# Performance work log

Hardware: AMD Instinct MI355X
Metric: run time of the kernel (lower is better)

The kernel has to match this reference:

```python
import jax, jax.numpy as jnp
import numpy as np

B, N_PER, P_PER = 64, 64, 2016   # graphs, nodes/graph, pairs/graph (C(64,2))
IN_DIM, HID, OUT = 64, 128, 10
EDGE_P = 0.125


def _build_graph_structures():
    """Integer preprocessing replicating build_2sets_from_embeddings's
    combinatorics (pairs, iso_type source, triangle-based 2-set edges)."""
    rng = np.random.default_rng(0)
    n, b = N_PER, B
    A = rng.random((b, n, n)) < EDGE_P
    A = np.triu(A, 1)
    A = A | A.transpose(0, 2, 1)                      # symmetric, no self loops
    gs, us, vs = np.nonzero(A)                        # directed edges, both dirs
    edge_index = np.stack([gs * n + us, gs * n + vs]).astype(np.int64)
    batch = np.repeat(np.arange(b), n).astype(np.int64)
    iu, iv = np.triu_indices(n, 1)                    # local pair (u<v) lists
    pidx = np.full((n, n), -1, np.int64)
    pidx[iu, iv] = np.arange(P_PER)
    pidx[iv, iu] = np.arange(P_PER)                   # symmetric lookup = sorted()
    pair_u = (np.arange(b)[:, None] * n + iu[None, :]).ravel().astype(np.int64)
    pair_v = (np.arange(b)[:, None] * n + iv[None, :]).ravel().astype(np.int64)
    iso_type = A[:, iu, iv].astype(np.float32).ravel()[:, None]  # [B*P_PER,1]
    # 2-set edges: pair (u,v) -> sorted(v,w) and sorted(u,w) for every common
    # neighbor w of u and v (matches _build_2set_edges exactly)
    common = A[:, iu, :] & A[:, iv, :]                # (B, P_PER, n)
    g2, ps, ws = np.nonzero(common)
    u, v = iu[ps], iv[ps]
    d1 = pidx[v, ws]
    d2 = pidx[u, ws]
    src = np.concatenate([g2 * P_PER + ps, g2 * P_PER + ps])
    dst = np.concatenate([g2 * P_PER + d1, g2 * P_PER + d2])
    two_edges = np.stack([src, dst]).astype(np.int64)
    two_batch = np.repeat(np.arange(b), P_PER).astype(np.int64)
    return edge_index, batch, pair_u, pair_v, iso_type, two_edges, two_batch


def setup_inputs() -> dict:
    ei, batch, pu, pv, iso, te, tb = _build_graph_structures()
    key = jax.random.key(0)
    ks = jax.random.split(key, 16)
    w = lambda k, i, o: jax.random.normal(k, (i, o), jnp.float32) / np.float32(np.sqrt(i))
    two_in = 2 * HID + 1
    return {
        "x": jax.random.normal(ks[0], (B * N_PER, IN_DIM), jnp.float32),
        "g1_W1_0": w(ks[1], IN_DIM, HID), "g1_W2_0": w(ks[2], IN_DIM, HID),
        "g1_W1_1": w(ks[3], HID, HID),    "g1_W2_1": w(ks[4], HID, HID),
        "g1_W1_2": w(ks[5], HID, HID),    "g1_W2_2": w(ks[6], HID, HID),
        "k_W1_0": w(ks[7], two_in, HID),  "k_W2_0": w(ks[8], two_in, HID),
        "k_W1_1": w(ks[9], HID, HID),     "k_W2_1": w(ks[10], HID, HID),
        "c_W0": w(ks[11], 2 * HID, HID),  "c_b0": jnp.zeros((HID,), jnp.float32),
        "c_W1": w(ks[12], HID, OUT),      "c_b1": jnp.zeros((OUT,), jnp.float32),
        "iso_type": jnp.asarray(iso),
        "edge_index": jnp.asarray(ei), "batch": jnp.asarray(batch),
        "pair_u": jnp.asarray(pu), "pair_v": jnp.asarray(pv),
        "two_edges": jnp.asarray(te), "two_batch": jnp.asarray(tb),
    }


def _mp_layer(h, ei, W1, W2):
    # relu( h @ W1 + scatter_add_{dst}( h[src] @ W2 ) )  -- OneGNNLayer / KSetLayer
    msg = h[ei[0]] @ W2
    agg = jax.ops.segment_sum(msg, ei[1], num_segments=h.shape[0])
    return jax.nn.relu(h @ W1 + agg)


def reference(x, g1_W1_0, g1_W2_0, g1_W1_1, g1_W2_1, g1_W1_2, g1_W2_2,
              k_W1_0, k_W2_0, k_W1_1, k_W2_1,
              c_W0, c_b0, c_W1, c_b1,
              iso_type, edge_index, batch, pair_u, pair_v, two_edges, two_batch):
    h = _mp_layer(x, edge_index, g1_W1_0, g1_W2_0)
    h = _mp_layer(h, edge_index, g1_W1_1, g1_W2_1)
    h = _mp_layer(h, edge_index, g1_W1_2, g1_W2_2)
    graph_emb_1 = jax.ops.segment_sum(h, batch, num_segments=B)
    # 2-set features: [h_u, h_v, iso_type]  -> [P, 2H+1]
    two_x = jnp.concatenate([h[pair_u], h[pair_v], iso_type], axis=1)
    h2 = _mp_layer(two_x, two_edges, k_W1_0, k_W2_0)
    h2 = _mp_layer(h2, two_edges, k_W1_1, k_W2_1)
    graph_emb_2 = jax.ops.segment_sum(h2, two_batch, num_segments=B)
    combined = jnp.concatenate([graph_emb_1, graph_emb_2], axis=1)
    hc = jax.nn.relu(combined @ c_W0 + c_b0)   # Dropout(p=0.5) inactive in eval
    return hc @ c_W1 + c_b1
```

## Files before the change

kernel.cpp:

```cpp
#include <hip/hip_runtime.h>
#include <hip/hip_bf16.h>


typedef short s16x8 __attribute__((ext_vector_type(8)));
typedef float f32x4 __attribute__((ext_vector_type(4)));

__device__ __forceinline__ unsigned short f2bf(float f) {
  union { float f; unsigned u; } x; x.f = f;
  unsigned r = (x.u + 0x7fffu + ((x.u >> 16) & 1u)) >> 16;
  return (unsigned short)r;
}
__device__ __forceinline__ float bf2f(unsigned short h) {
  union { unsigned u; float f; } x; x.u = ((unsigned)h) << 16;
  return x.f;
}
__device__ __forceinline__ float4 ldbf4(const unsigned short* p) {
  ushort4 q = *(const ushort4*)p;
  return make_float4(bf2f(q.x), bf2f(q.y), bf2f(q.z), bf2f(q.w));
}
__device__ __forceinline__ void stbf4(unsigned short* p, float4 v) {
  ushort4 q;
  q.x = f2bf(v.x); q.y = f2bf(v.y); q.z = f2bf(v.z); q.w = f2bf(v.w);
  *(ushort4*)p = q;
}
__device__ __forceinline__ float4 ld4(const float* p) { return *(const float4*)p; }

template<int KCS, int ASTR>
__device__ __forceinline__ void mfma_dual_lds(
    const unsigned short* A, const unsigned short* Wfrag,
    f32x4 (&accA)[8], f32x4 (&accB)[8])
{
  const int lane = threadIdx.x & 63;
  const int wv = threadIdx.x >> 6;
  const int row = wv * 16 + (lane & 15);
  const int k0 = (lane >> 4) << 3;
  const unsigned short* ap = A + row * ASTR + k0;
  const unsigned short* wp = Wfrag + (size_t)lane * 8;
#pragma unroll
  for (int i = 0; i < 8; ++i) { accA[i] = (f32x4)0.f; accB[i] = (f32x4)0.f; }
#pragma unroll
  for (int kc = 0; kc < KCS; ++kc) {
    s16x8 af = *(const s16x8*)(ap + kc * 32);
#pragma unroll
    for (int nt = 0; nt < 8; ++nt) {
      s16x8 b0 = *(const s16x8*)(wp + ((size_t)((nt)*KCS + kc) << 9));
      s16x8 b1 = *(const s16x8*)(wp + ((size_t)((8 + nt) * KCS + kc) << 9));
      accA[nt] = __builtin_amdgcn_mfma_f32_16x16x32_bf16(af, b0, accA[nt], 0, 0, 0);
      accB[nt] = __builtin_amdgcn_mfma_f32_16x16x32_bf16(af, b1, accB[nt], 0, 0, 0);
    }
  }
}

__device__ __forceinline__ void epi_lds(const f32x4 (&accA)[8], const f32x4 (&accB)[8],
    unsigned short (*preS)[136], unsigned short (*msgS)[136])
{
  const int lane = threadIdx.x & 63;
  const int wv = threadIdx.x >> 6;
  const int col = lane & 15;
  const int r0 = wv * 16 + ((lane >> 4) << 2);
  __syncthreads();
#pragma unroll
  for (int nt = 0; nt < 8; ++nt)
#pragma unroll
    for (int r = 0; r < 4; ++r) {
      preS[r0 + r][nt * 16 + col] = f2bf(accA[nt][r]);
      msgS[r0 + r][nt * 16 + col] = f2bf(accB[nt][r]);
    }
  __syncthreads();
}

__device__ __forceinline__ void epi_global(const f32x4 (&accA)[8], const f32x4 (&accB)[8],
    unsigned short (*sOut)[136], unsigned short* Ca, unsigned short* Cb, long tile)
{
  const int tid = threadIdx.x;
  const int lane = tid & 63;
  const int wv = tid >> 6;
  const int col = lane & 15;
  const int r0 = wv * 16 + ((lane >> 4) << 2);
  const long rowBase = tile * 64;
#pragma unroll
  for (int sel = 0; sel < 2; ++sel) {
    __syncthreads();
#pragma unroll
    for (int nt = 0; nt < 8; ++nt) {
#pragma unroll
      for (int r = 0; r < 4; ++r)
        sOut[r0 + r][nt * 16 + col] = f2bf(sel ? accB[nt][r] : accA[nt][r]);
    }
    __syncthreads();
    unsigned short* C = sel ? Cb : Ca;
#pragma unroll
    for (int i = 0; i < 4; ++i) {
      int fi = tid + i * 256;
      int row = fi >> 4;
      int c8 = fi & 15;
      *(uint4*)(C + (rowBase + row) * 128 + c8 * 8) = *(uint4*)&sOut[row][c8 * 8];
    }
  }
}

struct NArgs {
  const float* x;
  const int* ei;
  const int* gstart;
  const unsigned short *Wf0, *Wf1, *Wf2, *Wf3, *Wf4;
  unsigned short *HU1, *HV1, *HU2, *HV2;
  float* ge1;
  int E1;
};

__global__ __launch_bounds__(256) void node_stage(NArgs a)
{
  __shared__ __align__(16) unsigned short hS[64][136];
  __shared__ __align__(16) unsigned short preS[64][136];
  __shared__ __align__(16) unsigned short msgS[64][136];
  __shared__ int ldeg[64], lcur[64], loff[65];
  __shared__ unsigned short ledge[1024];
  __shared__ float sge[128];

  const int b = blockIdx.x;
  const int t = threadIdx.x;
  const int base = b * 64;

  const int es = a.gstart[b], ee = a.gstart[b + 1];
  if (t < 64) ldeg[t] = 0;
  if (t < 128) sge[t] = 0.f;
  __syncthreads();
  for (int i = es + t; i < ee; i += 256)
    atomicAdd(&ldeg[a.ei[a.E1 + i] - base], 1);
  __syncthreads();
  if (t < 64) {
    int v = ldeg[t], s = v;
#pragma unroll
    for (int d = 1; d < 64; d <<= 1) {
      int o = __shfl_up(s, d, 64);
      if (t >= d) s += o;
    }
    loff[t] = s - v;
    lcur[t] = s - v;
    if (t == 63) loff[64] = s;
  }
  unsigned short* xs = &preS[0][0];
  for (int i = t; i < 64 * 64; i += 256) {
    int r = i >> 6, c = i & 63;
    xs[r * 72 + c] = f2bf(a.x[(size_t)(base + r) * 64 + c]);
  }
  __syncthreads();
  for (int i = es + t; i < ee; i += 256) {
    int s = a.ei[i] - base, d = a.ei[a.E1 + i] - base;
    int pos = atomicAdd(&lcur[d], 1);
    ledge[pos] = (unsigned short)s;
  }
  __syncthreads();

  f32x4 accA[8], accB[8];
  const int grp = t >> 5, f = (t & 31) * 4;

  mfma_dual_lds<2, 72>(xs, a.Wf0, accA, accB);
  epi_lds(accA, accB, preS, msgS);
  for (int r = grp; r < 64; r += 8) {
    float4 acc = ldbf4(&preS[r][f]);
    int j1 = loff[r + 1];
    for (int j = loff[r]; j < j1; ++j) {
      float4 m = ldbf4(&msgS[ledge[j]][f]);
      acc.x += m.x; acc.y += m.y; acc.z += m.z; acc.w += m.w;
    }
    stbf4(&hS[r][f], make_float4(fmaxf(acc.x, 0.f), fmaxf(acc.y, 0.f),
                                 fmaxf(acc.z, 0.f), fmaxf(acc.w, 0.f)));
  }
  __syncthreads();

  mfma_dual_lds<4, 136>(&hS[0][0], a.Wf1, accA, accB);
  epi_lds(accA, accB, preS, msgS);
  for (int r = grp; r < 64; r += 8) {
    float4 acc = ldbf4(&preS[r][f]);
    int j1 = loff[r + 1];
    for (int j = loff[r]; j < j1; ++j) {
      float4 m = ldbf4(&msgS[ledge[j]][f]);
      acc.x += m.x; acc.y += m.y; acc.z += m.z; acc.w += m.w;
    }
    stbf4(&hS[r][f], make_float4(fmaxf(acc.x, 0.f), fmaxf(acc.y, 0.f),
                                 fmaxf(acc.z, 0.f), fmaxf(acc.w, 0.f)));
  }
  __syncthreads();

  mfma_dual_lds<4, 136>(&hS[0][0], a.Wf2, accA, accB);
  epi_lds(accA, accB, preS, msgS);
  {
    float4 g = make_float4(0.f, 0.f, 0.f, 0.f);
    for (int r = grp; r < 64; r += 8) {
      float4 acc = ldbf4(&preS[r][f]);
      int j1 = loff[r + 1];
      for (int j = loff[r]; j < j1; ++j) {
        float4 m = ldbf4(&msgS[ledge[j]][f]);
        acc.x += m.x; acc.y += m.y; acc.z += m.z; acc.w += m.w;
      }
      float4 o = make_float4(fmaxf(acc.x, 0.f), fmaxf(acc.y, 0.f),
                             fmaxf(acc.z, 0.f), fmaxf(acc.w, 0.f));
      stbf4(&hS[r][f], o);
      g.x += o.x; g.y += o.y; g.z += o.z; g.w += o.w;
    }
    atomicAdd(&sge[f + 0], g.x);
    atomicAdd(&sge[f + 1], g.y);
    atomicAdd(&sge[f + 2], g.z);
    atomicAdd(&sge[f + 3], g.w);
  }
  __syncthreads();
  if (t < 128) a.ge1[b * 128 + t] = sge[t];

  mfma_dual_lds<4, 136>(&hS[0][0], a.Wf3, accA, accB);
  epi_global(accA, accB, preS, a.HU1, a.HU2, b);
  mfma_dual_lds<4, 136>(&hS[0][0], a.Wf4, accA, accB);
  epi_global(accA, accB, preS, a.HV1, a.HV2, b);
}

struct PrepArgs {
  const float* wa[6];
  const float* wb[6];
  unsigned short* Wf[6];
  float* ge2;
  const int* te; int E2;
  int* degP;
  const int* ei; int E1;
  int* gstart;
  int nCnt;
};

__global__ void prep(PrepArgs p)
{
  int bb = blockIdx.x, t = threadIdx.x;
  if (bb < 88) {
    int gid = bb * 256 + t;
    if (gid < 22528) {
      int pi, local, kcs, kclog;
      if (gid < 2048) { pi = 0; local = gid; kcs = 2; kclog = 1; }
      else { int r = gid - 2048; pi = 1 + (r >> 12); local = r & 4095; kcs = 4; kclog = 2; }
      int lane = local & 63;
      int t1 = local >> 6;
      int kc = t1 & (kcs - 1);
      int t2 = t1 >> kclog;
      int nt = t2 & 7;
      int wsel = t2 >> 3;
      const float* W = wsel ? p.wb[pi] : p.wa[pi];
      int k0 = kc * 32 + ((lane >> 4) << 3);
      int n = nt * 16 + (lane & 15);
      unsigned short tmp[8];
#pragma unroll
      for (int j = 0; j < 8; ++j) tmp[j] = f2bf(W[(size_t)(k0 + j) * 128 + n]);
      *(uint4*)(p.Wf[pi] + (size_t)local * 8) = *(uint4*)tmp;
    }
  } else if (bb < 120) {
    int i = (bb - 88) * 256 + t;
    if (i < 8192) p.ge2[i] = 0.f;
  } else if (bb < 120 + p.nCnt) {
    int e = (bb - 120) * 256 + t;
    if (e < p.E2) atomicAdd(&p.degP[p.te[p.E2 + e]], 1);
  } else {
    int e = (bb - 120 - p.nCnt) * 256 + t;
    if (e <= p.E1) {
      int ge = (e < p.E1) ? (p.ei[e] >> 6) : 64;
      int gp = (e > 0) ? (p.ei[e - 1] >> 6) : -1;
      for (int g = gp + 1; g <= ge; ++g) p.gstart[g] = e;
    }
  }
}

__global__ __launch_bounds__(256) void scan_reduce(const int* __restrict__ deg,
                                                   int* __restrict__ bsum, int n)
{
  __shared__ int s[256];
  int b = blockIdx.x, t = threadIdx.x;
  int base = b * 1024;
  int v = 0;
#pragma unroll
  for (int i = 0; i < 4; ++i) {
    int idx = base + t + i * 256;
    if (idx < n) v += deg[idx];
  }
  s[t] = v;
  __syncthreads();
  for (int d = 128; d > 0; d >>= 1) {
    if (t < d) s[t] += s[t + d];
    __syncthreads();
  }
  if (t == 0) bsum[b] = s[0];
}

__global__ __launch_bounds__(1024) void scan_partials(int* __restrict__ bsum, int nb)
{
  __shared__ int s[1024];
  int t = threadIdx.x;
  s[t] = (t < nb) ? bsum[t] : 0;
  __syncthreads();
  for (int d = 1; d < 1024; d <<= 1) {
    int v = (t >= d) ? s[t - d] : 0;
    __syncthreads();
    s[t] += v;
    __syncthreads();
  }
  if (t < nb) bsum[t] = (t == 0) ? 0 : s[t - 1];
  if (t == 1023) bsum[nb] = s[1023];
}

__global__ __launch_bounds__(256) void scan_final(const int* __restrict__ deg,
                                                  const int* __restrict__ bsum,
                                                  int* __restrict__ off,
                                                  int* __restrict__ cur, int n, int nb)
{
  __shared__ int s[256];
  int b = blockIdx.x, t = threadIdx.x;
  int base = b * 1024 + t * 4;
  int v0 = 0, v1 = 0, v2 = 0, v3 = 0;
  if (base + 0 < n) v0 = deg[base + 0];
  if (base + 1 < n) v1 = deg[base + 1];
  if (base + 2 < n) v2 = deg[base + 2];
  if (base + 3 < n) v3 = deg[base + 3];
  s[t] = v0 + v1 + v2 + v3;
  __syncthreads();
  for (int d = 1; d < 256; d <<= 1) {
    int v = (t >= d) ? s[t - d] : 0;
    __syncthreads();
    s[t] += v;
    __syncthreads();
  }
  int run = bsum[b] + ((t == 0) ? 0 : s[t - 1]);
  if (base + 0 < n) { off[base + 0] = run; cur[base + 0] = run; run += v0; }
  if (base + 1 < n) { off[base + 1] = run; cur[base + 1] = run; run += v1; }
  if (base + 2 < n) { off[base + 2] = run; cur[base + 2] = run; run += v2; }
  if (base + 3 < n) { off[base + 3] = run; cur[base + 3] = run; run += v3; }
  if (b == 0 && t == 0) off[n] = bsum[nb];
}

__global__ void csr_fill_pair(const int* __restrict__ te, int E2,
                              const int* __restrict__ pu, const int* __restrict__ pv,
                              const float* __restrict__ iso,
                              int* __restrict__ curP, int4* __restrict__ recP)
{
  int e = blockIdx.x * 256 + threadIdx.x;
  if (e >= E2) return;
  int s = te[e], d = te[E2 + e];
  int pos = atomicAdd(&curP[d], 1);
  recP[pos] = make_int4(pu[s], pv[s], __float_as_int(iso[s]), s);
}

__global__ __launch_bounds__(256) void gemm_dual_mfma4(
    const unsigned short* __restrict__ A, const unsigned short* __restrict__ Wfrag,
    unsigned short* __restrict__ Ca, unsigned short* __restrict__ Cb)
{
  __shared__ __align__(16) unsigned short sA[64][136];
  const int tid = threadIdx.x;
  const int lane = tid & 63;
  const int wv = tid >> 6;
  const long rowBase = (long)blockIdx.x * 64;

  f32x4 accA[8], accB[8];
#pragma unroll
  for (int i = 0; i < 8; ++i) { accA[i] = (f32x4)0.f; accB[i] = (f32x4)0.f; }

  const unsigned short* aptr =
      A + (size_t)(rowBase + wv * 16 + (lane & 15)) * 128 + ((lane >> 4) << 3);
  const unsigned short* wptr = Wfrag + (size_t)lane * 8;

#pragma unroll
  for (int kc = 0; kc < 4; ++kc) {
    s16x8 af = *(const s16x8*)(aptr + kc * 32);
#pragma unroll
    for (int nt = 0; nt < 8; ++nt) {
      s16x8 b0 = *(const s16x8*)(wptr + ((size_t)((nt)*4 + kc) << 9));
      s16x8 b1 = *(const s16x8*)(wptr + ((size_t)((8 + nt) * 4 + kc) << 9));
      accA[nt] = __builtin_amdgcn_mfma_f32_16x16x32_bf16(af, b0, accA[nt], 0, 0, 0);
      accB[nt] = __builtin_amdgcn_mfma_f32_16x16x32_bf16(af, b1, accB[nt], 0, 0, 0);
    }
  }
  epi_global(accA, accB, sA, Ca, Cb, blockIdx.x);
}

__global__ __launch_bounds__(256) void gather_two0_bf(
    const unsigned short* __restrict__ HU1, const unsigned short* __restrict__ HV1,
    const unsigned short* __restrict__ HU2, const unsigned short* __restrict__ HV2,
    const float* __restrict__ iso,
    const float* __restrict__ w1iso, const float* __restrict__ w2iso,
    const int* __restrict__ pu, const int* __restrict__ pv,
    const int* __restrict__ off, const int4* __restrict__ rec,
    unsigned short* __restrict__ out, int P)
{
  int p = blockIdx.x * 8 + (threadIdx.x >> 5);
  if (p >= P) return;
  int f = (threadIdx.x & 31) * 4;
  float4 wi1 = ld4(w1iso + f);
  float4 wi2 = ld4(w2iso + f);
  int u0 = pu[p], v0 = pv[p];
  float is0 = iso[p];
  float4 a = ldbf4(HU1 + (size_t)u0 * 128 + f);
  float4 b = ldbf4(HV1 + (size_t)v0 * 128 + f);
  float4 acc;
  acc.x = a.x + b.x + is0 * wi1.x;
  acc.y = a.y + b.y + is0 * wi1.y;
  acc.z = a.z + b.z + is0 * wi1.z;
  acc.w = a.w + b.w + is0 * wi1.w;
  int j = off[p], e1 = off[p + 1];
  for (; j + 1 < e1; j += 2) {
    int4 r0 = rec[j], r1 = rec[j + 1];
    float4 mu0 = ldbf4(HU2 + (size_t)r0.x * 128 + f);
    float4 mv0 = ldbf4(HV2 + (size_t)r0.y * 128 + f);
    float4 mu1 = ldbf4(HU2 + (size_t)r1.x * 128 + f);
    float4 mv1 = ldbf4(HV2 + (size_t)r1.y * 128 + f);
    float i0 = __int_as_float(r0.z), i1 = __int_as_float(r1.z);
    acc.x += mu0.x + mv0.x + i0 * wi2.x + mu1.x + mv1.x + i1 * wi2.x;
    acc.y += mu0.y + mv0.y + i0 * wi2.y + mu1.y + mv1.y + i1 * wi2.y;
    acc.z += mu0.z + mv0.z + i0 * wi2.z + mu1.z + mv1.z + i1 * wi2.z;
    acc.w += mu0.w + mv0.w + i0 * wi2.w + mu1.w + mv1.w + i1 * wi2.w;
  }
  if (j < e1) {
    int4 r0 = rec[j];
    float4 mu0 = ldbf4(HU2 + (size_t)r0.x * 128 + f);
    float4 mv0 = ldbf4(HV2 + (size_t)r0.y * 128 + f);
    float i0 = __int_as_float(r0.z);
    acc.x += mu0.x + mv0.x + i0 * wi2.x;
    acc.y += mu0.y + mv0.y + i0 * wi2.y;
    acc.z += mu0.z + mv0.z + i0 * wi2.z;
    acc.w += mu0.w + mv0.w + i0 * wi2.w;
  }
  stbf4(out + (size_t)p * 128 + f,
        make_float4(fmaxf(acc.x, 0.f), fmaxf(acc.y, 0.f),
                    fmaxf(acc.z, 0.f), fmaxf(acc.w, 0.f)));
}

__global__ __launch_bounds__(256) void gather_rec_segsum(
    const unsigned short* __restrict__ pre, const unsigned short* __restrict__ msg,
    const int* __restrict__ off, const int4* __restrict__ rec,
    float* __restrict__ ge2, int ppg)
{
  __shared__ float sF[128];
  int t = threadIdx.x;
  if (t < 128) sF[t] = 0.f;
  __syncthreads();
  int g = blockIdx.x >> 4;
  int sub = blockIdx.x & 15;
  int r0 = g * ppg + sub * 126;
  int grp = t >> 5;
  int f = (t & 31) * 4;
  float4 gacc = make_float4(0.f, 0.f, 0.f, 0.f);
  for (int rr = grp; rr < 126; rr += 8) {
    int r = r0 + rr;
    float4 acc = ldbf4(pre + (size_t)r * 128 + f);
    int j = off[r], e1 = off[r + 1];
    for (; j + 1 < e1; j += 2) {
      int4 q0 = rec[j], q1 = rec[j + 1];
      float4 m0 = ldbf4(msg + (size_t)q0.w * 128 + f);
      float4 m1 = ldbf4(msg + (size_t)q1.w * 128 + f);
      acc.x += m0.x + m1.x; acc.y += m0.y + m1.y;
      acc.z += m0.z + m1.z; acc.w += m0.w + m1.w;
    }
    if (j < e1) {
      int4 q0 = rec[j];
      float4 m0 = ldbf4(msg + (size_t)q0.w * 128 + f);
      acc.x += m0.x; acc.y += m0.y; acc.z += m0.z; acc.w += m0.w;
    }
    gacc.x += fmaxf(acc.x, 0.f); gacc.y += fmaxf(acc.y, 0.f);
    gacc.z += fmaxf(acc.z, 0.f); gacc.w += fmaxf(acc.w, 0.f);
  }
  atomicAdd(&sF[f + 0], gacc.x);
  atomicAdd(&sF[f + 1], gacc.y);
  atomicAdd(&sF[f + 2], gacc.z);
  atomicAdd(&sF[f + 3], gacc.w);
  __syncthreads();
  if (t < 128) atomicAdd(&ge2[g * 128 + t], sF[t]);
}

__global__ void classifier(const float* __restrict__ ge1, const float* __restrict__ ge2,
                           const float* __restrict__ W0, const float* __restrict__ b0,
                           const float* __restrict__ W1, const float* __restrict__ b1,
                           float* __restrict__ out)
{
  __shared__ float comb[256];
  __shared__ float hc[128];
  int g = blockIdx.x, t = threadIdx.x;
  comb[t]       = ge1[g * 128 + t];
  comb[t + 128] = ge2[g * 128 + t];
  __syncthreads();
  float s = b0[t];
  for (int k = 0; k < 256; ++k) s += comb[k] * W0[k * 128 + t];
  hc[t] = fmaxf(s, 0.f);
  __syncthreads();
  if (t < 10) {
    float s2 = b1[t];
    for (int k = 0; k < 128; ++k) s2 += hc[k] * W1[k * 10 + t];
    out[g * 10 + t] = s2;
  }
}

extern "C" void kernel_launch(void* const* d_in, const int* in_sizes, int n_in,
                              void* d_out, int out_size, void* d_ws, size_t ws_size,
                              hipStream_t stream)
{
  (void)n_in; (void)out_size; (void)ws_size;
  const float* x       = (const float*)d_in[0];
  const float* g1_W1_0 = (const float*)d_in[1];
  const float* g1_W2_0 = (const float*)d_in[2];
  const float* g1_W1_1 = (const float*)d_in[3];
  const float* g1_W2_1 = (const float*)d_in[4];
  const float* g1_W1_2 = (const float*)d_in[5];
  const float* g1_W2_2 = (const float*)d_in[6];
  const float* k_W1_0  = (const float*)d_in[7];
  const float* k_W2_0  = (const float*)d_in[8];
  const float* k_W1_1  = (const float*)d_in[9];
  const float* k_W2_1  = (const float*)d_in[10];
  const float* c_W0    = (const float*)d_in[11];
  const float* c_b0    = (const float*)d_in[12];
  const float* c_W1    = (const float*)d_in[13];
  const float* c_b1    = (const float*)d_in[14];
  const float* iso     = (const float*)d_in[15];
  const int*   ei      = (const int*)d_in[16];
  const int*   pu      = (const int*)d_in[18];
  const int*   pv      = (const int*)d_in[19];
  const int*   te      = (const int*)d_in[20];

  const int N  = in_sizes[0] / 64;
  const int E1 = in_sizes[16] / 2;
  const int P  = in_sizes[18];
  const int E2 = in_sizes[20] / 2;
  const int B  = 64;
  const int ppg = P / B;

  const size_t NH = (size_t)N * 128;
  const size_t PH = (size_t)P * 128;

  float* ge1 = (float*)d_ws;
  float* ge2 = ge1 + 8192;
  unsigned short* HU1 = (unsigned short*)(ge2 + 8192);
  unsigned short* HV1 = HU1 + NH;
  unsigned short* HU2 = HV1 + NH;
  unsigned short* HV2 = HU2 + NH;
  unsigned short* H2   = HV2 + NH;
  unsigned short* PRE2 = H2 + PH;
  unsigned short* MSG2 = PRE2 + PH;
  unsigned short* Wf0  = MSG2 + PH;
  unsigned short* Wf1  = Wf0 + 16384;
  unsigned short* Wf2  = Wf1 + 32768;
  unsigned short* Wf3  = Wf2 + 32768;
  unsigned short* Wf4  = Wf3 + 32768;
  unsigned short* Wf5  = Wf4 + 32768;

  size_t ipOff = ((size_t)((char*)(Wf5 + 32768) - (char*)d_ws) + 15) & ~(size_t)15;
  int4* recP   = (int4*)((char*)d_ws + ipOff);
  int* degP    = (int*)(recP + E2);
  int* offP    = degP + P;
  int* curP    = offP + P + 1;
  int* bsumP   = curP + P;
  int* gstartN = bsumP + 128;

  const int nbP  = (P + 1023) / 1024;
  const int nCnt = (E2 + 255) / 256;
  const int nBnd = (E1 + 256) / 256;

  hipMemsetAsync(degP, 0, (size_t)P * 4, stream);

  PrepArgs pa;
  pa.wa[0] = g1_W1_0;           pa.wb[0] = g1_W2_0;
  pa.wa[1] = g1_W1_1;           pa.wb[1] = g1_W2_1;
  pa.wa[2] = g1_W1_2;           pa.wb[2] = g1_W2_2;
  pa.wa[3] = k_W1_0;            pa.wb[3] = k_W2_0;
  pa.wa[4] = k_W1_0 + 128*128;  pa.wb[4] = k_W2_0 + 128*128;
  pa.wa[5] = k_W1_1;            pa.wb[5] = k_W2_1;
  pa.Wf[0] = Wf0; pa.Wf[1] = Wf1; pa.Wf[2] = Wf2;
  pa.Wf[3] = Wf3; pa.Wf[4] = Wf4; pa.Wf[5] = Wf5;
  pa.ge2 = ge2; pa.te = te; pa.E2 = E2; pa.degP = degP;
  pa.ei = ei; pa.E1 = E1; pa.gstart = gstartN; pa.nCnt = nCnt;
  prep<<<120 + nCnt + nBnd, 256, 0, stream>>>(pa);

  scan_reduce<<<nbP, 256, 0, stream>>>(degP, bsumP, P);
  scan_partials<<<1, 1024, 0, stream>>>(bsumP, nbP);
  scan_final<<<nbP, 256, 0, stream>>>(degP, bsumP, offP, curP, P, nbP);
  csr_fill_pair<<<nCnt, 256, 0, stream>>>(te, E2, pu, pv, iso, curP, recP);

  NArgs na;
  na.x = x; na.ei = ei; na.gstart = gstartN; na.E1 = E1;
  na.Wf0 = Wf0; na.Wf1 = Wf1; na.Wf2 = Wf2; na.Wf3 = Wf3; na.Wf4 = Wf4;
  na.HU1 = HU1; na.HU2 = HU2; na.HV1 = HV1; na.HV2 = HV2;
  na.ge1 = ge1;
  node_stage<<<B, 256, 0, stream>>>(na);

  gather_two0_bf<<<(P + 7) / 8, 256, 0, stream>>>(HU1, HV1, HU2, HV2, iso,
                                                  k_W1_0 + 256 * 128, k_W2_0 + 256 * 128,
                                                  pu, pv, offP, recP, H2, P);

  gemm_dual_mfma4<<<P / 64, 256, 0, stream>>>(H2, Wf5, PRE2, MSG2);

  gather_rec_segsum<<<B * 16, 256, 0, stream>>>(PRE2, MSG2, offP, recP, ge2, ppg);

  classifier<<<B, 128, 0, stream>>>(ge1, ge2, c_W0, c_b0, c_W1, c_b1, (float*)d_out);
}
```

Before: 319.1 us.

## Fuse 2-set layer-0 gather into MFMA GEMM via LDS; finer-grained segsum blocks

The first 2-set layer's gather-and-relu now writes each 64-row tile into shared memory, and the dual MFMA GEMM reads it from there in the same kernel. This drops the H2 intermediate's global write and read plus one launch. Separately, the final gather/segment-sum kernel now runs one pair per 32-thread group across P/8 blocks, interleaved across graphs, instead of 126-row loops in 1024 blocks. This raises parallelism but adds more shared-memory and global atomics per pair.

```diff
diff --git a/kernel.cpp b/kernel.cpp
--- a/kernel.cpp
+++ b/kernel.cpp
@@ -343,90 +343,71 @@
   recP[pos] = make_int4(pu[s], pv[s], __float_as_int(iso[s]), s);
 }
 
-__global__ __launch_bounds__(256) void gemm_dual_mfma4(
-    const unsigned short* __restrict__ A, const unsigned short* __restrict__ Wfrag,
-    unsigned short* __restrict__ Ca, unsigned short* __restrict__ Cb)
-{
-  __shared__ __align__(16) unsigned short sA[64][136];
-  const int tid = threadIdx.x;
-  const int lane = tid & 63;
-  const int wv = tid >> 6;
-  const long rowBase = (long)blockIdx.x * 64;
+struct TGArgs {
+  const unsigned short *HU1, *HV1, *HU2, *HV2;
+  const float *iso, *w1iso, *w2iso;
+  const int *pu, *pv, *off;
+  const int4* rec;
+  const unsigned short* Wf5;
+  unsigned short *PRE2, *MSG2;
+};
+
+__global__ __launch_bounds__(256) void two0_gemm(TGArgs a)
+{
+  __shared__ __align__(16) unsigned short hS[64][136];
+  const int t = threadIdx.x;
+  const long tile = blockIdx.x;
+  const int grp = t >> 5, f = (t & 31) * 4;
+  float4 wi1 = ld4(a.w1iso + f);
+  float4 wi2 = ld4(a.w2iso + f);
+
+#pragma unroll 2
+  for (int rr = 0; rr < 8; ++rr) {
+    int rl = grp * 8 + rr;
+    int p = (int)(tile * 64 + rl);
+    int u0 = a.pu[p], v0 = a.pv[p];
+    float is0 = a.iso[p];
+    float4 xx = ldbf4(a.HU1 + (size_t)u0 * 128 + f);
+    float4 yy = ldbf4(a.HV1 + (size_t)v0 * 128 + f);
+    float4 acc;
+    acc.x = xx.x + yy.x + is0 * wi1.x;
+    acc.y = xx.y + yy.y + is0 * wi1.y;
+    acc.z = xx.z + yy.z + is0 * wi1.z;
+    acc.w = xx.w + yy.w + is0 * wi1.w;
+    int j = a.off[p], e1 = a.off[p + 1];
+    for (; j + 1 < e1; j += 2) {
+      int4 r0 = a.rec[j], r1 = a.rec[j + 1];
+      float4 mu0 = ldbf4(a.HU2 + (size_t)r0.x * 128 + f);
+      float4 mv0 = ldbf4(a.HV2 + (size_t)r0.y * 128 + f);
+      float4 mu1 = ldbf4(a.HU2 + (size_t)r1.x * 128 + f);
+      float4 mv1 = ldbf4(a.HV2 + (size_t)r1.y * 128 + f);
+      float i0 = __int_as_float(r0.z), i1 = __int_as_float(r1.z);
+      acc.x += mu0.x + mv0.x + i0 * wi2.x + mu1.x + mv1.x + i1 * wi2.x;
+      acc.y += mu0.y + mv0.y + i0 * wi2.y + mu1.y + mv1.y + i1 * wi2.y;
+      acc.z += mu0.z + mv0.z + i0 * wi2.z + mu1.z + mv1.z + i1 * wi2.z;
+      acc.w += mu0.w + mv0.w + i0 * wi2.w + mu1.w + mv1.w + i1 * wi2.w;
+    }
+    if (j < e1) {
+      int4 r0 = a.rec[j];
+      float4 mu0 = ldbf4(a.HU2 + (size_t)r0.x * 128 + f);
+      float4 mv0 = ldbf4(a.HV2 + (size_t)r0.y * 128 + f);
+      float i0 = __int_as_float(r0.z);
+      acc.x += mu0.x + mv0.x + i0 * wi2.x;
+      acc.y += mu0.y + mv0.y + i0 * wi2.y;
+      acc.z += mu0.z + mv0.z + i0 * wi2.z;
+      acc.w += mu0.w + mv0.w + i0 * wi2.w;
+    }
+    stbf4(&hS[rl][f], make_float4(fmaxf(acc.x, 0.f), fmaxf(acc.y, 0.f),
+                                  fmaxf(acc.z, 0.f), fmaxf(acc.w, 0.f)));
+  }
+  __syncthreads();
 
   f32x4 accA[8], accB[8];
-#pragma unroll
-  for (int i = 0; i < 8; ++i) { accA[i] = (f32x4)0.f; accB[i] = (f32x4)0.f; }
-
-  const unsigned short* aptr =
-      A + (size_t)(rowBase + wv * 16 + (lane & 15)) * 128 + ((lane >> 4) << 3);
-  const unsigned short* wptr = Wfrag + (size_t)lane * 8;
-
-#pragma unroll
-  for (int kc = 0; kc < 4; ++kc) {
-    s16x8 af = *(const s16x8*)(aptr + kc * 32);
-#pragma unroll
-    for (int nt = 0; nt < 8; ++nt) {
-      s16x8 b0 = *(const s16x8*)(wptr + ((size_t)((nt)*4 + kc) << 9));
-      s16x8 b1 = *(const s16x8*)(wptr + ((size_t)((8 + nt) * 4 + kc) << 9));
-      accA[nt] = __builtin_amdgcn_mfma_f32_16x16x32_bf16(af, b0, accA[nt], 0, 0, 0);
-      accB[nt] = __builtin_amdgcn_mfma_f32_16x16x32_bf16(af, b1, accB[nt], 0, 0, 0);
-    }
-  }
-  epi_global(accA, accB, sA, Ca, Cb, blockIdx.x);
-}
-
-__global__ __launch_bounds__(256) void gather_two0_bf(
-    const unsigned short* __restrict__ HU1, const unsigned short* __restrict__ HV1,
-    const unsigned short* __restrict__ HU2, const unsigned short* __restrict__ HV2,
-    const float* __restrict__ iso,
-    const float* __restrict__ w1iso, const float* __restrict__ w2iso,
-    const int* __restrict__ pu, const int* __restrict__ pv,
-    const int* __restrict__ off, const int4* __restrict__ rec,
-    unsigned short* __restrict__ out, int P)
-{
-  int p = blockIdx.x * 8 + (threadIdx.x >> 5);
-  if (p >= P) return;
-  int f = (threadIdx.x & 31) * 4;
-  float4 wi1 = ld4(w1iso + f);
-  float4 wi2 = ld4(w2iso + f);
-  int u0 = pu[p], v0 = pv[p];
-  float is0 = iso[p];
-  float4 a = ldbf4(HU1 + (size_t)u0 * 128 + f);
-  float4 b = ldbf4(HV1 + (size_t)v0 * 128 + f);
-  float4 acc;
-  acc.x = a.x + b.x + is0 * wi1.x;
-  acc.y = a.y + b.y + is0 * wi1.y;
-  acc.z = a.z + b.z + is0 * wi1.z;
-  acc.w = a.w + b.w + is0 * wi1.w;
-  int j = off[p], e1 = off[p + 1];
-  for (; j + 1 < e1; j += 2) {
-    int4 r0 = rec[j], r1 = rec[j + 1];
-    float4 mu0 = ldbf4(HU2 + (size_t)r0.x * 128 + f);
-    float4 mv0 = ldbf4(HV2 + (size_t)r0.y * 128 + f);
-    float4 mu1 = ldbf4(HU2 + (size_t)r1.x * 128 + f);
-    float4 mv1 = ldbf4(HV2 + (size_t)r1.y * 128 + f);
-    float i0 = __int_as_float(r0.z), i1 = __int_as_float(r1.z);
-    acc.x += mu0.x + mv0.x + i0 * wi2.x + mu1.x + mv1.x + i1 * wi2.x;
-    acc.y += mu0.y + mv0.y + i0 * wi2.y + mu1.y + mv1.y + i1 * wi2.y;
-    acc.z += mu0.z + mv0.z + i0 * wi2.z + mu1.z + mv1.z + i1 * wi2.z;
-    acc.w += mu0.w + mv0.w + i0 * wi2.w + mu1.w + mv1.w + i1 * wi2.w;
-  }
-  if (j < e1) {
-    int4 r0 = rec[j];
-    float4 mu0 = ldbf4(HU2 + (size_t)r0.x * 128 + f);
-    float4 mv0 = ldbf4(HV2 + (size_t)r0.y * 128 + f);
-    float i0 = __int_as_float(r0.z);
-    acc.x += mu0.x + mv0.x + i0 * wi2.x;
-    acc.y += mu0.y + mv0.y + i0 * wi2.y;
-    acc.z += mu0.z + mv0.z + i0 * wi2.z;
-    acc.w += mu0.w + mv0.w + i0 * wi2.w;
-  }
-  stbf4(out + (size_t)p * 128 + f,
-        make_float4(fmaxf(acc.x, 0.f), fmaxf(acc.y, 0.f),
-                    fmaxf(acc.z, 0.f), fmaxf(acc.w, 0.f)));
-}
-
-__global__ __launch_bounds__(256) void gather_rec_segsum(
+  mfma_dual_lds<4, 136>(&hS[0][0], a.Wf5, accA, accB);
+  epi_global(accA, accB, hS, a.PRE2, a.MSG2, tile);
+}
+
+__global__ __launch_bounds__(256) void gather_segsum8(
     const unsigned short* __restrict__ pre, const unsigned short* __restrict__ msg,
     const int* __restrict__ off, const int4* __restrict__ rec,
     float* __restrict__ ge2, int ppg)
@@ -435,35 +416,32 @@
   int t = threadIdx.x;
   if (t < 128) sF[t] = 0.f;
   __syncthreads();
-  int g = blockIdx.x >> 4;
-  int sub = blockIdx.x & 15;
-  int r0 = g * ppg + sub * 126;
-  int grp = t >> 5;
+  int bpg = ppg >> 3;
+  int c = blockIdx.x & 7;
+  int j = blockIdx.x >> 3;
+  int g = c + 8 * (j / bpg);
+  int sub = j % bpg;
+  int r = g * ppg + sub * 8 + (t >> 5);
   int f = (t & 31) * 4;
-  float4 gacc = make_float4(0.f, 0.f, 0.f, 0.f);
-  for (int rr = grp; rr < 126; rr += 8) {
-    int r = r0 + rr;
-    float4 acc = ldbf4(pre + (size_t)r * 128 + f);
-    int j = off[r], e1 = off[r + 1];
-    for (; j + 1 < e1; j += 2) {
-      int4 q0 = rec[j], q1 = rec[j + 1];
-      float4 m0 = ldbf4(msg + (size_t)q0.w * 128 + f);
-      float4 m1 = ldbf4(msg + (size_t)q1.w * 128 + f);
-      acc.x += m0.x + m1.x; acc.y += m0.y + m1.y;
-      acc.z += m0.z + m1.z; acc.w += m0.w + m1.w;
-    }
-    if (j < e1) {
-      int4 q0 = rec[j];
-      float4 m0 = ldbf4(msg + (size_t)q0.w * 128 + f);
-      acc.x += m0.x; acc.y += m0.y; acc.z += m0.z; acc.w += m0.w;
-    }
-    gacc.x += fmaxf(acc.x, 0.f); gacc.y += fmaxf(acc.y, 0.f);
-    gacc.z += fmaxf(acc.z, 0.f); gacc.w += fmaxf(acc.w, 0.f);
-  }
-  atomicAdd(&sF[f + 0], gacc.x);
-  atomicAdd(&sF[f + 1], gacc.y);
-  atomicAdd(&sF[f + 2], gacc.z);
-  atomicAdd(&sF[f + 3], gacc.w);
+
+  float4 acc = ldbf4(pre + (size_t)r * 128 + f);
+  int jj = off[r], e1 = off[r + 1];
+  for (; jj + 1 < e1; jj += 2) {
+    int4 q0 = rec[jj], q1 = rec[jj + 1];
+    float4 m0 = ldbf4(msg + (size_t)q0.w * 128 + f);
+    float4 m1 = ldbf4(msg + (size_t)q1.w * 128 + f);
+    acc.x += m0.x + m1.x; acc.y += m0.y + m1.y;
+    acc.z += m0.z + m1.z; acc.w += m0.w + m1.w;
+  }
+  if (jj < e1) {
+    int4 q0 = rec[jj];
+    float4 m0 = ldbf4(msg + (size_t)q0.w * 128 + f);
+    acc.x += m0.x; acc.y += m0.y; acc.z += m0.z; acc.w += m0.w;
+  }
+  atomicAdd(&sF[f + 0], fmaxf(acc.x, 0.f));
+  atomicAdd(&sF[f + 1], fmaxf(acc.y, 0.f));
+  atomicAdd(&sF[f + 2], fmaxf(acc.z, 0.f));
+  atomicAdd(&sF[f + 3], fmaxf(acc.w, 0.f));
   __syncthreads();
   if (t < 128) atomicAdd(&ge2[g * 128 + t], sF[t]);
 }
@@ -532,8 +510,7 @@
   unsigned short* HV1 = HU1 + NH;
   unsigned short* HU2 = HV1 + NH;
   unsigned short* HV2 = HU2 + NH;
-  unsigned short* H2   = HV2 + NH;
-  unsigned short* PRE2 = H2 + PH;
+  unsigned short* PRE2 = HV2 + NH;
   unsigned short* MSG2 = PRE2 + PH;
   unsigned short* Wf0  = MSG2 + PH;
   unsigned short* Wf1  = Wf0 + 16384;
@@ -581,13 +558,14 @@
   na.ge1 = ge1;
   node_stage<<<B, 256, 0, stream>>>(na);
 
-  gather_two0_bf<<<(P + 7) / 8, 256, 0, stream>>>(HU1, HV1, HU2, HV2, iso,
-                                                  k_W1_0 + 256 * 128, k_W2_0 + 256 * 128,
-                                                  pu, pv, offP, recP, H2, P);
-
-  gemm_dual_mfma4<<<P / 64, 256, 0, stream>>>(H2, Wf5, PRE2, MSG2);
-
-  gather_rec_segsum<<<B * 16, 256, 0, stream>>>(PRE2, MSG2, offP, recP, ge2, ppg);
+  TGArgs ta;
+  ta.HU1 = HU1; ta.HV1 = HV1; ta.HU2 = HU2; ta.HV2 = HV2;
+  ta.iso = iso; ta.w1iso = k_W1_0 + 256 * 128; ta.w2iso = k_W2_0 + 256 * 128;
+  ta.pu = pu; ta.pv = pv; ta.off = offP; ta.rec = recP;
+  ta.Wf5 = Wf5; ta.PRE2 = PRE2; ta.MSG2 = MSG2;
+  two0_gemm<<<P / 64, 256, 0, stream>>>(ta);
+
+  gather_segsum8<<<P / 8, 256, 0, stream>>>(PRE2, MSG2, offP, recP, ge2, ppg);
 
   classifier<<<B, 128, 0, stream>>>(ge1, ge2, c_W0, c_b0, c_W1, c_b1, (float*)d_out);
 }
```

Measured after the change: 363.9 us. 1.14x slower.
